# Kernel optimization log

Measured on AMD Instinct MI355X. Metric: run time of the kernel, lower is better.

The kernel has to match this reference:

```python
import jax, jax.numpy as jnp
import numpy as np

N = 729        # problem variables
B = 8          # batch
K = 32         # mixing rank (hard-coded in MixingFunc)
NB = 40        # number of symmetry-basis matrices
MAX_ITER = 10  # coordinate-descent sweeps


def setup_inputs() -> dict:
    key = jax.random.key(0)
    ks = jax.random.split(key, 7)
    coeff = jax.random.normal(ks[0], (NB,), jnp.float32)
    upper = jax.random.normal(ks[1], (N,), jnp.float32)
    basis = jax.random.normal(ks[2], (NB, N, N), jnp.float32)
    z = jax.random.uniform(ks[3], (B, N), jnp.float32)
    is_input = jax.random.randint(ks[4], (B, N), 0, 2).astype(jnp.int32)
    v_init_raw = jax.random.normal(ks[5], (B, N + 1, K), jnp.float32)
    # random permutation of the N non-truth variables (indices 1..N), as in satnet init
    perm = (jax.random.permutation(ks[6], N) + 1).astype(jnp.int32)
    return dict(coeff=coeff, upper=upper, basis=basis, z=z,
                is_input=is_input, v_init_raw=v_init_raw, perm=perm)


def _build_C(coeff, upper, basis):
    # BasisFunc.forward: C = [[0, upper^T], [upper, sum_b coeff_b * basis_b]]
    center = jnp.einsum('b,bij->ij', coeff, basis)              # (N, N)
    top = jnp.concatenate([jnp.zeros((1,), upper.dtype), upper])[None, :]  # (1, N+1)
    bottom = jnp.concatenate([upper[:, None], center], axis=1)  # (N, N+1)
    return jnp.concatenate([top, bottom], axis=0)               # (N+1, N+1)


def _init_V(v_raw, z_full):
    # SATNet init: v0 = random unit truth direction; each v_i is placed on the
    # cone around v0 at angle pi*z_i using a random orthogonal direction.
    v0 = v_raw[:, 0] / jnp.linalg.norm(v_raw[:, 0], axis=-1, keepdims=True)  # (B, K)
    dot = jnp.einsum('bnk,bk->bn', v_raw, v0)
    u = v_raw - dot[..., None] * v0[:, None, :]
    u = u / jnp.maximum(jnp.linalg.norm(u, axis=-1, keepdims=True), 1e-8)
    c = jnp.cos(jnp.pi * z_full)[..., None]
    s = jnp.sin(jnp.pi * z_full)[..., None]
    V = -c * v0[:, None, :] + s * u                              # (B, N+1, K)
    V = V.at[:, 0].set(v0)                                       # truth vector pinned
    return V


def _mix(C, V, is_input_full, perm):
    # SATNet mixing coordinate descent: for each free variable i,
    #   g_i = sum_j C[j,i] v_j - C[i,i] v_i ;  v_i <- -g_i / ||g_i||
    Cdiag = jnp.diagonal(C)
    free = (is_input_full == 0)                                  # (B, N+1)

    def coord_step(V, i):
        g = jnp.einsum('j,bjk->bk', C[:, i], V) - Cdiag[i] * V[:, i]  # (B, K)
        gn = jnp.linalg.norm(g, axis=-1, keepdims=True)
        vnew = -g / jnp.maximum(gn, 1e-8)
        V = V.at[:, i].set(jnp.where(free[:, i][:, None], vnew, V[:, i]))
        return V, None

    def sweep(V, _):
        V, _ = jax.lax.scan(coord_step, V, perm)
        return V, None

    V, _ = jax.lax.scan(jax.checkpoint(sweep), V, None, length=MAX_ITER)
    return V


def reference(coeff, upper, basis, z, is_input, v_init_raw, perm):
    Bn = z.shape[0]
    C = _build_C(coeff, upper, basis)
    z_full = jnp.concatenate([jnp.ones((Bn, 1), z.dtype), z], axis=1)
    ii_full = jnp.concatenate(
        [jnp.ones((Bn, 1), is_input.dtype), is_input], axis=1)
    V = _init_V(v_init_raw, z_full)
    V = _mix(C, V, ii_full, perm)
    v0 = V[:, 0]
    cosang = jnp.clip(-jnp.einsum('bnk,bk->bn', V, v0), -1.0 + 1e-6, 1.0 - 1e-6)
    zo = jnp.arccos(cosang) / jnp.pi
    z_out = jnp.where(ii_full == 1, z_full, zo)
    return z_out[:, 1:]
```

## Files before the change

kernel.cpp:

```cpp
#include <hip/hip_runtime.h>

#define NN   729
#define NF   730
#define BV   8
#define KK   32
#define NBAS 40
#define MAXIT 10
#define PI_F 3.14159265358979323846f

#define MTH   512
#define BT    16
#define AST   448
#define CPST  20

typedef float v2f __attribute__((ext_vector_type(2)));

__device__ __forceinline__ void fma4(float4& w, float c, const float4& d) {
    w.x = fmaf(c, d.x, w.x); w.y = fmaf(c, d.y, w.y);
    w.z = fmaf(c, d.z, w.z); w.w = fmaf(c, d.w, w.w);
}

__global__ void build_C_kernel(const float* __restrict__ coeff,
                               const float* __restrict__ upper,
                               const float* __restrict__ basis,
                               float* __restrict__ Ct) {
    int idx = blockIdx.x * blockDim.x + threadIdx.x;
    if (idx >= NF * NF) return;
    int i = idx / NF, j = idx - i * NF;
    float val;
    if (i == 0) {
        val = (j == 0) ? 0.f : upper[j - 1];
    } else if (j == 0) {
        val = upper[i - 1];
    } else {
        float acc = 0.f;
        const float* bp = basis + (size_t)(i - 1) * NN + (j - 1);
        #pragma unroll 8
        for (int b = 0; b < NBAS; ++b)
            acc = fmaf(coeff[b], bp[(size_t)b * NN * NN], acc);
        val = acc;
    }
    Ct[(size_t)j * NF + i] = val;
}

__global__ void init_V_kernel(const float* __restrict__ z,
                              const float* __restrict__ vraw,
                              float* __restrict__ V) {
    int g = threadIdx.x >> 5;
    int k = threadIdx.x & 31;
    int row = blockIdx.x * 8 + g;
    int b = row / NF, n = row - b * NF;
    const float* vr = vraw + (size_t)b * NF * KK;

    float v0 = vr[k];
    float s2 = v0 * v0;
    #pragma unroll
    for (int off = 16; off; off >>= 1) s2 += __shfl_xor(s2, off, 32);
    v0 = v0 / sqrtf(s2);

    float vn = vr[(size_t)n * KK + k];
    float d = vn * v0;
    #pragma unroll
    for (int off = 16; off; off >>= 1) d += __shfl_xor(d, off, 32);
    float u = vn - d * v0;
    float un2 = u * u;
    #pragma unroll
    for (int off = 16; off; off >>= 1) un2 += __shfl_xor(un2, off, 32);
    u = u / fmaxf(sqrtf(un2), 1e-8f);

    float zf = (n == 0) ? 1.f : z[b * NN + (n - 1)];
    float c = cosf(PI_F * zf), s = sinf(PI_F * zf);
    float outv = -c * v0 + s * u;
    if (n == 0) outv = v0;
    V[((size_t)b * NF + n) * KK + k] = outv;
}

__global__ void build_act_kernel(const int* __restrict__ is_input,
                                 const int* __restrict__ perm,
                                 int* __restrict__ act, int* __restrict__ nA_arr) {
    int b = blockIdx.x, l = threadIdx.x;
    int base = 0;
    for (int c = 0; c < (NN + 63) / 64; ++c) {
        int idx = c * 64 + l;
        bool f = false; int pi = 0;
        if (idx < NN) { pi = perm[idx]; f = (is_input[b * NN + pi - 1] == 0); }
        unsigned long long m = __ballot(f);
        int pos = __popcll(m & ((1ull << l) - 1ull));
        if (f && base + pos < AST) act[b * AST + base + pos] = pi;
        base += __popcll(m);
    }
    if (base > AST) base = AST;
    if (l == 0) nA_arr[b] = base;
    for (int p = base + l; p < AST; p += 64) act[b * AST + p] = 0;
}

__global__ void gather_CactT_kernel(const float* __restrict__ Ct,
                                    const int* __restrict__ act,
                                    float* __restrict__ CactT) {
    int a = blockIdx.x, b = blockIdx.y;
    __shared__ int acts[AST];
    for (int i = threadIdx.x; i < AST; i += blockDim.x) acts[i] = act[b * AST + i];
    __syncthreads();
    const float* src = Ct + (size_t)acts[a] * NF;
    float* dst = CactT + ((size_t)b * AST + a) * AST;
    for (int t = threadIdx.x; t < AST; t += blockDim.x)
        dst[t] = src[acts[t]];
}

__global__ void init_W_kernel(const float* __restrict__ Ct,
                              const int* __restrict__ act,
                              const int* __restrict__ nA_arr,
                              const float* __restrict__ V,
                              float* __restrict__ Wc,
                              float* __restrict__ Vact) {
    int b = blockIdx.y;
    int a = blockIdx.x * 8 + (threadIdx.x >> 5);
    int k = threadIdx.x & 31;
    int nA = nA_arr[b];
    float w = 0.f;
    int ra = act[b * AST + a];
    float vv = V[((size_t)b * NF + ra) * KK + k];
    if (a < nA) {
        const float* ctr = Ct + (size_t)ra * NF;
        const float* vb = V + (size_t)b * NF * KK + k;
        float acc = 0.f;
        for (int j = 0; j < NF; ++j)
            acc = fmaf(ctr[j], vb[(size_t)j * KK], acc);
        w = acc - ctr[ra] * vv;
    }
    Wc[((size_t)b * AST + a) * KK + k] = w;
    Vact[((size_t)b * AST + a) * KK + k] = vv;
}

__device__ __forceinline__ float rowsum16(float x) {
    int y;
    y = __builtin_amdgcn_update_dpp(0, __float_as_int(x), 0x121, 0xF, 0xF, false);
    x += __int_as_float(y);
    y = __builtin_amdgcn_update_dpp(0, __float_as_int(x), 0x122, 0xF, 0xF, false);
    x += __int_as_float(y);
    y = __builtin_amdgcn_update_dpp(0, __float_as_int(x), 0x124, 0xF, 0xF, false);
    x += __int_as_float(y);
    y = __builtin_amdgcn_update_dpp(0, __float_as_int(x), 0x128, 0xF, 0xF, false);
    x += __int_as_float(y);
    return x;
}

__global__ __launch_bounds__(MTH, 2)
void mix_kernel(const float* __restrict__ CactT_g,
                const float* __restrict__ Wc_g,
                const float* __restrict__ Vact_g,
                const int* __restrict__ act_g,
                const int* __restrict__ nA_arr,
                const int* __restrict__ is_input,
                const float* __restrict__ z,
                const float* __restrict__ Vg,
                float* __restrict__ out) {
    __shared__ __align__(16) float V_c[AST * KK];
    __shared__ __align__(16) float cpanel[2][AST * CPST];
    __shared__ __align__(16) float dv_s[2][BT * KK];
    __shared__ __align__(16) float gpub[BT * KK];
    __shared__ __align__(16) float cblk_s[2][BT * BT];
    __shared__ __align__(16) float cmini_s[2][BT * BT];
    __shared__ float Cd_s[AST];
    __shared__ int   slot_s[NF];

    int b = blockIdx.x, tid = threadIdx.x;
    const float* CT = CactT_g + (size_t)b * AST * AST;
    const float* Vact = Vact_g + (size_t)b * AST * KK;
    int nA = nA_arr[b];
    int nblkp = (nA + BT - 1) / BT;
    if (nblkp < 2) nblkp = 2;
    int nAp = nblkp * BT;
    int totB = MAXIT * nblkp;

    int wid = tid >> 6;
    int l64 = tid & 63;
    int lane = tid - 64;
    int kq = lane & 7;
    int rslot = lane >> 3;
    int kp = tid & 15;

    for (int idx = tid; idx < AST * 8; idx += MTH)
        ((float4*)V_c)[idx] = ((const float4*)Vact)[idx];
    if (tid < AST) Cd_s[tid] = CT[(size_t)tid * AST + tid];
    if (tid < nA) slot_s[act_g[b * AST + tid]] = tid;
    if (tid < 256) {
        int t = tid >> 4, u = tid & 15;
        cblk_s[0][t * BT + u] = CT[(size_t)u * AST + t];
    }
    float4 w[8];
    #pragma unroll
    for (int p = 0; p < 8; ++p) {
        float4 zz = {0.f, 0.f, 0.f, 0.f};
        w[p] = zz;
        if (wid >= 1)
            w[p] = *(const float4*)&Wc_g[((size_t)b * AST + rslot + 56 * p) * KK + 4 * kq];
    }
    __syncthreads();

    for (int bi = 0; bi < totB; ++bi) {
        int blk = bi % nblkp, s0 = blk * BT;
        int pblk = (bi - 1 + nblkp) % nblkp, sp0 = pblk * BT;
        int cb = bi & 1, pv = cb ^ 1;
        int sn0 = ((bi + 1) % nblkp) * BT;

        float4 st0, st1, st2, st3;
        if (wid >= 1) {
            const float* srcp = CT + (size_t)lane * AST + s0;
            st0 = *(const float4*)(srcp);
            st1 = *(const float4*)(srcp + 4);
            st2 = *(const float4*)(srcp + 8);
            st3 = *(const float4*)(srcp + 12);
            #pragma unroll
            for (int p = 0; p < 8; ++p) {
                int a = rslot + 56 * p;
                if ((a >> 4) == blk) {
                    int u = a - s0;
                    if (bi > 0) {
                        #pragma unroll
                        for (int q = 0; q < 4; ++q) {
                            float4 cm = *(const float4*)&cmini_s[cb][u * BT + 4 * q];
                            float4 d;
                            d = *(const float4*)&dv_s[pv][(4*q+0) * KK + 4 * kq];
                            fma4(w[p], cm.x, d);
                            d = *(const float4*)&dv_s[pv][(4*q+1) * KK + 4 * kq];
                            fma4(w[p], cm.y, d);
                            d = *(const float4*)&dv_s[pv][(4*q+2) * KK + 4 * kq];
                            fma4(w[p], cm.z, d);
                            d = *(const float4*)&dv_s[pv][(4*q+3) * KK + 4 * kq];
                            fma4(w[p], cm.w, d);
                        }
                    }
                    *(float4*)&gpub[u * KK + 4 * kq] = w[p];
                }
            }
        }
        __syncthreads();

        if (wid == 0) {
            float g0[BT], g1[BT], vo0[BT], vo1[BT];
            #pragma unroll
            for (int u = 0; u < BT; ++u) {
                v2f gv = *(const v2f*)&gpub[u * KK + 2 * kp];
                g0[u] = gv.x; g1[u] = gv.y;
                v2f vv = *(const v2f*)&V_c[(s0 + u) * KK + 2 * kp];
                vo0[u] = vv.x; vo1[u] = vv.y;
            }
            #pragma unroll
            for (int u = 0; u < BT; ++u) {
                int s = s0 + u;
                float n2 = fmaf(g0[u], g0[u], g1[u] * g1[u]);
                n2 = rowsum16(n2);
                float inv = -__builtin_amdgcn_rsqf(fmaxf(n2, 1e-16f));
                float msk = (s < nA) ? 1.f : 0.f;
                float d0 = fmaf(g0[u], inv, -vo0[u]) * msk;
                float d1 = fmaf(g1[u], inv, -vo1[u]) * msk;
                if (tid < 16) {
                    v2f dv2; dv2.x = d0; dv2.y = d1;
                    *(v2f*)&dv_s[cb][u * KK + 2 * kp] = dv2;
                    v2f vn2; vn2.x = vo0[u] + d0; vn2.y = vo1[u] + d1;
                    *(v2f*)&V_c[s * KK + 2 * kp] = vn2;
                }
                #pragma unroll
                for (int u2 = u + 1; u2 < BT; ++u2) {
                    float c = cblk_s[cb][u * BT + u2];
                    g0[u2] = fmaf(c, d0, g0[u2]);
                    g1[u2] = fmaf(c, d1, g1[u2]);
                }
            }
        } else {
            if (bi > 0) {
                #pragma unroll
                for (int h = 0; h < 2; ++h) {
                    float4 dvv[8];
                    #pragma unroll
                    for (int t = 0; t < 8; ++t)
                        dvv[t] = *(const float4*)&dv_s[pv][(8 * h + t) * KK + 4 * kq];
                    #pragma unroll
                    for (int p = 0; p < 8; ++p) {
                        int a = rslot + 56 * p;
                        if (a < nAp && (a >> 4) != blk) {
                            float4 cA = *(const float4*)&cpanel[cb][a * CPST + 8 * h];
                            float4 cB = *(const float4*)&cpanel[cb][a * CPST + 8 * h + 4];
                            fma4(w[p], cA.x, dvv[0]);
                            fma4(w[p], cA.y, dvv[1]);
                            fma4(w[p], cA.z, dvv[2]);
                            fma4(w[p], cA.w, dvv[3]);
                            fma4(w[p], cB.x, dvv[4]);
                            fma4(w[p], cB.y, dvv[5]);
                            fma4(w[p], cB.z, dvv[6]);
                            fma4(w[p], cB.w, dvv[7]);
                        }
                    }
                }
                #pragma unroll
                for (int p = 0; p < 8; ++p) {
                    int a = rslot + 56 * p;
                    if ((a >> 4) == pblk) {
                        float4 dd = *(const float4*)&dv_s[pv][(a - sp0) * KK + 4 * kq];
                        fma4(w[p], -Cd_s[a], dd);
                    }
                }
            }
            {
                float* dst = &cpanel[pv][lane * CPST];
                *(float4*)(dst)      = st0;
                *(float4*)(dst + 4)  = st1;
                *(float4*)(dst + 8)  = st2;
                *(float4*)(dst + 12) = st3;
            }
            if (wid == 7) {
                {
                    int u = l64 & 15, q = l64 >> 4;
                    float4 v = *(const float4*)&CT[(size_t)(sn0 + u) * AST + s0 + 4 * q];
                    *(float4*)&cmini_s[pv][u * BT + 4 * q] = v;
                }
                {
                    int u = l64 & 15, q = l64 >> 4;
                    float4 v = *(const float4*)&CT[(size_t)(sn0 + u) * AST + sn0 + 4 * q];
                    cblk_s[pv][(4 * q + 0) * BT + u] = v.x;
                    cblk_s[pv][(4 * q + 1) * BT + u] = v.y;
                    cblk_s[pv][(4 * q + 2) * BT + u] = v.z;
                    cblk_s[pv][(4 * q + 3) * BT + u] = v.w;
                }
            }
        }
        __syncthreads();
    }

    int k = tid & 31, r = tid >> 5;
    float v0k = Vg[(size_t)b * NF * KK + k];
    for (int n = 1 + r; n <= NN; n += 16) {
        int ii = is_input[b * NN + n - 1];
        float res;
        if (ii == 1) {
            res = z[b * NN + n - 1];
        } else {
            int a = slot_s[n];
            float dot = V_c[a * KK + k] * v0k;
            #pragma unroll
            for (int off = 16; off; off >>= 1) dot += __shfl_xor(dot, off, 32);
            float ca = fminf(fmaxf(-dot, -1.f + 1e-6f), 1.f - 1e-6f);
            res = acosf(ca) * (1.f / PI_F);
        }
        if (k == 0) out[b * NN + n - 1] = res;
    }
}

extern "C" void kernel_launch(void* const* d_in, const int* in_sizes, int n_in,
                              void* d_out, int out_size, void* d_ws, size_t ws_size,
                              hipStream_t stream) {
    const float* coeff    = (const float*)d_in[0];
    const float* upper    = (const float*)d_in[1];
    const float* basis    = (const float*)d_in[2];
    const float* z        = (const float*)d_in[3];
    const int*   is_input = (const int*)d_in[4];
    const float* vraw     = (const float*)d_in[5];
    const int*   perm     = (const int*)d_in[6];
    float* out = (float*)d_out;

    float* ws    = (float*)d_ws;
    float* Ct    = ws;
    float* V     = Ct + (size_t)NF * NF;
    float* CactT = V + (size_t)BV * NF * KK;
    float* Wc    = CactT + (size_t)BV * AST * AST;
    float* Vact  = Wc + (size_t)BV * AST * KK;
    int*   act   = (int*)(Vact + (size_t)BV * AST * KK);
    int*   nAa   = act + BV * AST;

    build_C_kernel<<<dim3((NF * NF + 255) / 256), dim3(256), 0, stream>>>(coeff, upper, basis, Ct);
    init_V_kernel<<<dim3(730), dim3(256), 0, stream>>>(z, vraw, V);
    build_act_kernel<<<dim3(BV), dim3(64), 0, stream>>>(is_input, perm, act, nAa);
    gather_CactT_kernel<<<dim3(AST, BV), dim3(256), 0, stream>>>(Ct, act, CactT);
    init_W_kernel<<<dim3(AST / 8, BV), dim3(256), 0, stream>>>(Ct, act, nAa, V, Wc, Vact);
    mix_kernel<<<dim3(BV), dim3(MTH), 0, stream>>>(CactT, Wc, Vact, act, nAa, is_input, z, V, out);
}
```

Before: 743.0 us.

## Read C panel directly from global/L2 instead of staging through LDS

Removes the double-buffered shared-memory C panel and mini-block staging. The off-block gradient update and the same-block correction now load C coefficients straight from global memory, with a software register double-buffer across rows. A padding shared array is added, apparently to keep LDS usage, and therefore occupancy, at its previous level. This trades LDS stores, LDS reads and a prefetch for global loads that now sit on the critical path of each block step, so their latency is exposed unless L2 hits hide it.

```diff
diff --git a/kernel.cpp b/kernel.cpp
--- a/kernel.cpp
+++ b/kernel.cpp
@@ -11,7 +11,6 @@
 #define MTH   512
 #define BT    16
 #define AST   448
-#define CPST  20
 
 typedef float v2f __attribute__((ext_vector_type(2)));
 
@@ -156,13 +155,12 @@
                 const float* __restrict__ Vg,
                 float* __restrict__ out) {
     __shared__ __align__(16) float V_c[AST * KK];
-    __shared__ __align__(16) float cpanel[2][AST * CPST];
     __shared__ __align__(16) float dv_s[2][BT * KK];
     __shared__ __align__(16) float gpub[BT * KK];
     __shared__ __align__(16) float cblk_s[2][BT * BT];
-    __shared__ __align__(16) float cmini_s[2][BT * BT];
     __shared__ float Cd_s[AST];
     __shared__ int   slot_s[NF];
+    __shared__ float ldspad[3200];
 
     int b = blockIdx.x, tid = threadIdx.x;
     const float* CT = CactT_g + (size_t)b * AST * AST;
@@ -188,6 +186,7 @@
         int t = tid >> 4, u = tid & 15;
         cblk_s[0][t * BT + u] = CT[(size_t)u * AST + t];
     }
+    if (tid == 0) ldspad[3199] = 0.f;
     float4 w[8];
     #pragma unroll
     for (int p = 0; p < 8; ++p) {
@@ -204,32 +203,35 @@
         int cb = bi & 1, pv = cb ^ 1;
         int sn0 = ((bi + 1) % nblkp) * BT;
 
-        float4 st0, st1, st2, st3;
         if (wid >= 1) {
-            const float* srcp = CT + (size_t)lane * AST + s0;
-            st0 = *(const float4*)(srcp);
-            st1 = *(const float4*)(srcp + 4);
-            st2 = *(const float4*)(srcp + 8);
-            st3 = *(const float4*)(srcp + 12);
             #pragma unroll
             for (int p = 0; p < 8; ++p) {
                 int a = rslot + 56 * p;
                 if ((a >> 4) == blk) {
                     int u = a - s0;
                     if (bi > 0) {
-                        #pragma unroll
-                        for (int q = 0; q < 4; ++q) {
-                            float4 cm = *(const float4*)&cmini_s[cb][u * BT + 4 * q];
-                            float4 d;
-                            d = *(const float4*)&dv_s[pv][(4*q+0) * KK + 4 * kq];
-                            fma4(w[p], cm.x, d);
-                            d = *(const float4*)&dv_s[pv][(4*q+1) * KK + 4 * kq];
-                            fma4(w[p], cm.y, d);
-                            d = *(const float4*)&dv_s[pv][(4*q+2) * KK + 4 * kq];
-                            fma4(w[p], cm.z, d);
-                            d = *(const float4*)&dv_s[pv][(4*q+3) * KK + 4 * kq];
-                            fma4(w[p], cm.w, d);
-                        }
+                        const float* cr = CT + (size_t)a * AST + sp0;
+                        float4 c0 = *(const float4*)(cr);
+                        float4 c1 = *(const float4*)(cr + 4);
+                        float4 c2 = *(const float4*)(cr + 8);
+                        float4 c3 = *(const float4*)(cr + 12);
+                        float4 d;
+                        d = *(const float4*)&dv_s[pv][0  * KK + 4 * kq]; fma4(w[p], c0.x, d);
+                        d = *(const float4*)&dv_s[pv][1  * KK + 4 * kq]; fma4(w[p], c0.y, d);
+                        d = *(const float4*)&dv_s[pv][2  * KK + 4 * kq]; fma4(w[p], c0.z, d);
+                        d = *(const float4*)&dv_s[pv][3  * KK + 4 * kq]; fma4(w[p], c0.w, d);
+                        d = *(const float4*)&dv_s[pv][4  * KK + 4 * kq]; fma4(w[p], c1.x, d);
+                        d = *(const float4*)&dv_s[pv][5  * KK + 4 * kq]; fma4(w[p], c1.y, d);
+                        d = *(const float4*)&dv_s[pv][6  * KK + 4 * kq]; fma4(w[p], c1.z, d);
+                        d = *(const float4*)&dv_s[pv][7  * KK + 4 * kq]; fma4(w[p], c1.w, d);
+                        d = *(const float4*)&dv_s[pv][8  * KK + 4 * kq]; fma4(w[p], c2.x, d);
+                        d = *(const float4*)&dv_s[pv][9  * KK + 4 * kq]; fma4(w[p], c2.y, d);
+                        d = *(const float4*)&dv_s[pv][10 * KK + 4 * kq]; fma4(w[p], c2.z, d);
+                        d = *(const float4*)&dv_s[pv][11 * KK + 4 * kq]; fma4(w[p], c2.w, d);
+                        d = *(const float4*)&dv_s[pv][12 * KK + 4 * kq]; fma4(w[p], c3.x, d);
+                        d = *(const float4*)&dv_s[pv][13 * KK + 4 * kq]; fma4(w[p], c3.y, d);
+                        d = *(const float4*)&dv_s[pv][14 * KK + 4 * kq]; fma4(w[p], c3.z, d);
+                        d = *(const float4*)&dv_s[pv][15 * KK + 4 * kq]; fma4(w[p], c3.w, d);
                     }
                     *(float4*)&gpub[u * KK + 4 * kq] = w[p];
                 }
@@ -269,6 +271,14 @@
                 }
             }
         } else {
+            if (wid == 7) {
+                int u = l64 & 15, q = l64 >> 4;
+                float4 v = *(const float4*)&CT[(size_t)(sn0 + u) * AST + sn0 + 4 * q];
+                cblk_s[pv][(4 * q + 0) * BT + u] = v.x;
+                cblk_s[pv][(4 * q + 1) * BT + u] = v.y;
+                cblk_s[pv][(4 * q + 2) * BT + u] = v.z;
+                cblk_s[pv][(4 * q + 3) * BT + u] = v.w;
+            }
             if (bi > 0) {
                 #pragma unroll
                 for (int h = 0; h < 2; ++h) {
@@ -276,20 +286,31 @@
                     #pragma unroll
                     for (int t = 0; t < 8; ++t)
                         dvv[t] = *(const float4*)&dv_s[pv][(8 * h + t) * KK + 4 * kq];
+                    float4 cA0, cB0, cA1, cB1;
+                    {
+                        const float* cr = CT + (size_t)rslot * AST + sp0 + 8 * h;
+                        cA0 = *(const float4*)(cr);
+                        cB0 = *(const float4*)(cr + 4);
+                    }
                     #pragma unroll
                     for (int p = 0; p < 8; ++p) {
                         int a = rslot + 56 * p;
+                        if (p < 7) {
+                            const float* cr = CT + (size_t)(a + 56) * AST + sp0 + 8 * h;
+                            if (p & 1) { cA0 = *(const float4*)(cr); cB0 = *(const float4*)(cr + 4); }
+                            else       { cA1 = *(const float4*)(cr); cB1 = *(const float4*)(cr + 4); }
+                        }
+                        float4 ca = (p & 1) ? cA1 : cA0;
+                        float4 cbq = (p & 1) ? cB1 : cB0;
                         if (a < nAp && (a >> 4) != blk) {
-                            float4 cA = *(const float4*)&cpanel[cb][a * CPST + 8 * h];
-                            float4 cB = *(const float4*)&cpanel[cb][a * CPST + 8 * h + 4];
-                            fma4(w[p], cA.x, dvv[0]);
-                            fma4(w[p], cA.y, dvv[1]);
-                            fma4(w[p], cA.z, dvv[2]);
-                            fma4(w[p], cA.w, dvv[3]);
-                            fma4(w[p], cB.x, dvv[4]);
-                            fma4(w[p], cB.y, dvv[5]);
-                            fma4(w[p], cB.z, dvv[6]);
-                            fma4(w[p], cB.w, dvv[7]);
+                            fma4(w[p], ca.x,  dvv[0]);
+                            fma4(w[p], ca.y,  dvv[1]);
+                            fma4(w[p], ca.z,  dvv[2]);
+                            fma4(w[p], ca.w,  dvv[3]);
+                            fma4(w[p], cbq.x, dvv[4]);
+                            fma4(w[p], cbq.y, dvv[5]);
+                            fma4(w[p], cbq.z, dvv[6]);
+                            fma4(w[p], cbq.w, dvv[7]);
                         }
                     }
                 }
@@ -300,28 +321,6 @@
                         float4 dd = *(const float4*)&dv_s[pv][(a - sp0) * KK + 4 * kq];
                         fma4(w[p], -Cd_s[a], dd);
                     }
-                }
-            }
-            {
-                float* dst = &cpanel[pv][lane * CPST];
-                *(float4*)(dst)      = st0;
-                *(float4*)(dst + 4)  = st1;
-                *(float4*)(dst + 8)  = st2;
-                *(float4*)(dst + 12) = st3;
-            }
-            if (wid == 7) {
-                {
-                    int u = l64 & 15, q = l64 >> 4;
-                    float4 v = *(const float4*)&CT[(size_t)(sn0 + u) * AST + s0 + 4 * q];
-                    *(float4*)&cmini_s[pv][u * BT + 4 * q] = v;
-                }
-                {
-                    int u = l64 & 15, q = l64 >> 4;
-                    float4 v = *(const float4*)&CT[(size_t)(sn0 + u) * AST + sn0 + 4 * q];
-                    cblk_s[pv][(4 * q + 0) * BT + u] = v.x;
-                    cblk_s[pv][(4 * q + 1) * BT + u] = v.y;
-                    cblk_s[pv][(4 * q + 2) * BT + u] = v.z;
-                    cblk_s[pv][(4 * q + 3) * BT + u] = v.w;
                 }
             }
         }
```

Result: no change. 738.8 us (-0.6%).
